# Kernel optimization log

Measured on AMD Instinct MI355X. Metric: run time of the kernel, lower is better.

Reference implementation:

```python
import jax, jax.numpy as jnp
import numpy as np

B, N, C = 4, 4096, 1024
H, D = 16, 64
EPS = 1e-6


def setup_inputs() -> dict:
    key = jax.random.key(0)
    ks = jax.random.split(key, 7)
    x = jax.random.normal(ks[0], (B, N, C), dtype=jnp.float32)
    # True = PAD (PyTorch convention)
    src_key_padding_mask = jax.random.randint(ks[1], (B, N), 0, 2).astype(jnp.bool_)
    s = 1.0 / np.sqrt(C)
    W_qkv = jax.random.uniform(ks[2], (3 * C, C), jnp.float32, -s, s)
    b_qkv = jax.random.uniform(ks[3], (3 * C,), jnp.float32, -s, s)
    W_out = jax.random.uniform(ks[4], (C, C), jnp.float32, -s, s)
    b_out = jax.random.uniform(ks[5], (C,), jnp.float32, -s, s)
    return {"x": x, "W_qkv": W_qkv, "b_qkv": b_qkv, "W_out": W_out,
            "b_out": b_out, "src_key_padding_mask": src_key_padding_mask}


def _phi(t):
    # elu(t) + 1  (alpha=1)
    return jnp.where(t > 0, t + 1.0, jnp.exp(t))


def reference(x, W_qkv, b_qkv, W_out, b_out, src_key_padding_mask):
    # qkv projection: [B,N,3C] -> [3,B,H,N,D]
    qkv = (x @ W_qkv.T + b_qkv).reshape(B, N, 3, H, D).transpose(2, 0, 3, 1, 4)
    q, k, v = qkv[0], qkv[1], qkv[2]
    qf = _phi(q)
    kf = _phi(k)
    valid = (~src_key_padding_mask).astype(kf.dtype)[:, None, :, None]  # [B,1,N,1]
    kf = kf * valid
    v = v * valid
    # kv state: [B,H,D,D]; z: [B,H,D]
    kv = jnp.einsum('bhnd,bhne->bhde', kf, v)
    z = kf.sum(axis=2)
    y_num = jnp.einsum('bhnd,bhde->bhne', qf, kv)      # [B,H,N,D]
    y_den = jnp.einsum('bhnd,bhd->bhn', qf, z)          # [B,H,N]
    y_den = jnp.maximum(y_den, EPS)[..., None]
    y = (y_num / y_den).transpose(0, 2, 1, 3).reshape(B, N, C)
    return y @ W_out.T + b_out
```

## Files before the change

### kernel.cpp

```cpp
#include <hip/hip_runtime.h>
#include <math.h>

#define B_ 4
#define N_ 4096
#define C_ 1024
#define H_ 16
#define D_ 64
#define M_ (B_*N_)
#define GK 1024
#define NCH 8
#define CHROWS (N_/NCH)

typedef __attribute__((ext_vector_type(8))) _Float16 f16x8;
typedef __attribute__((ext_vector_type(4))) _Float16 f16x4;
typedef __attribute__((ext_vector_type(4))) float f32x4;

__device__ __forceinline__ float phi_f(float t) {
  return (t > 0.0f) ? (t + 1.0f) : __expf(t);
}

#define GLOAD(gp, lp) __builtin_amdgcn_global_load_lds( \
    (const __attribute__((address_space(1))) unsigned int*)(gp), \
    (__attribute__((address_space(3))) unsigned int*)(lp), 16, 0, 0)

#define BAR() __builtin_amdgcn_s_barrier()
#define WAITL0() asm volatile("s_waitcnt lgkmcnt(0)" ::: "memory")
#define WAITV6() asm volatile("s_waitcnt vmcnt(6)" ::: "memory")
#define WAITV0() asm volatile("s_waitcnt vmcnt(0)" ::: "memory")
#define PRIO1() __builtin_amdgcn_s_setprio(1)
#define PRIO0() __builtin_amdgcn_s_setprio(0)

__device__ __forceinline__ f32x4 mfma16h(f16x8 a, f16x8 b, f32x4 c) {
  return __builtin_amdgcn_mfma_f32_16x16x32_f16(a, b, c, 0, 0, 0);
}

__global__ __launch_bounds__(256) void mask_detect_k(const unsigned int* __restrict__ w,
                                                     int* __restrict__ flag) {
  __shared__ int notint, notflt;
  if (threadIdx.x == 0) { notint = 0; notflt = 0; }
  __syncthreads();
  int ni = 0, nf = 0;
  for (int i = threadIdx.x; i < 4096; i += 256) {
    unsigned int v = w[i];
    if (v > 1u) ni = 1;
    if (v != 0u && v != 0x3F800000u) nf = 1;
  }
  if (ni) atomicOr(&notint, 1);
  if (nf) atomicOr(&notflt, 1);
  __syncthreads();
  if (threadIdx.x == 0) *flag = (!notint) ? 0 : ((!notflt) ? 1 : 2);
}

__global__ __launch_bounds__(256) void mask_convert_k(const void* __restrict__ mask,
                                                      const int* __restrict__ flag,
                                                      float* __restrict__ valid) {
  int i = blockIdx.x * 256 + threadIdx.x;
  int f = *flag;
  int m;
  if (f == 0)      m = ((const int*)mask)[i] != 0;
  else if (f == 1) m = ((const float*)mask)[i] != 0.0f;
  else             m = ((const unsigned char*)mask)[i] != 0;
  valid[i] = m ? 0.0f : 1.0f;
}

__global__ __launch_bounds__(256) void conv_f16_k(const float* __restrict__ src,
                                                  _Float16* __restrict__ dst, int n4) {
  int i = blockIdx.x * 256 + threadIdx.x;
  if (i >= n4) return;
  float4 v = ((const float4*)src)[i];
  f16x4 h;
  h[0] = (_Float16)v.x; h[1] = (_Float16)v.y;
  h[2] = (_Float16)v.z; h[3] = (_Float16)v.w;
  ((f16x4*)dst)[i] = h;
}

__global__ __launch_bounds__(256) void split_f16_k(const float* __restrict__ src,
                                                   _Float16* __restrict__ h,
                                                   _Float16* __restrict__ l, int n4) {
  int i = blockIdx.x * 256 + threadIdx.x;
  if (i >= n4) return;
  float4 v = ((const float4*)src)[i];
  f16x4 hv, lv;
  float vs[4] = {v.x, v.y, v.z, v.w};
#pragma unroll
  for (int q = 0; q < 4; ++q) {
    _Float16 hh = (_Float16)vs[q];
    _Float16 ll = (_Float16)(vs[q] - (float)hh);
    hv[q] = hh; lv[q] = ll;
  }
  ((f16x4*)h)[i] = hv;
  ((f16x4*)l)[i] = lv;
}

template <int EPI>
__global__ __launch_bounds__(512, 2) void gemm256_k(
    const _Float16* __restrict__ A,
    const _Float16* __restrict__ Bh, const _Float16* __restrict__ Bl,
    const float* __restrict__ bias, const float* __restrict__ valid,
    float* __restrict__ qf, float* __restrict__ kf, float* __restrict__ vv,
    float* __restrict__ outp, int jb, int jshift) {
  __shared__ _Float16 lds[73728];
  const int tid = threadIdx.x;
  const int lane = tid & 63, w = tid >> 6;
  const int lm = lane & 15, lq = lane >> 4;
  const int wm = w >> 2, wj = w & 3;

  const int nwg = gridDim.x;
  const int q8 = nwg >> 3;
  const int wid = (blockIdx.x & 7) * q8 + (blockIdx.x >> 3);
  const int j_blk = wid & ((1 << jshift) - 1);
  const int m_blk = wid >> jshift;
  const int m0 = m_blk * 256;
  const int jg0 = jb + j_blk * 256;

  const size_t gA0 = (size_t)(m0 + w * 16 + lm) * GK + lq * 8;
  const size_t gA1 = gA0 + (size_t)128 * GK;
  const size_t gB0 = (size_t)(jg0 + w * 16 + lm) * GK + lq * 8;
  const size_t gB1 = gB0 + (size_t)128 * GK;

#pragma unroll
  for (int tt = 0; tt < 2; ++tt) {
    _Float16* sq = lds + tt * 24576;
    const size_t ks = (size_t)tt * 32;
    GLOAD(A + gA0 + ks, sq + w * 512);
    GLOAD(A + gA1 + ks, sq + 4096 + w * 512);
    GLOAD(Bh + gB0 + ks, sq + 8192 + w * 512);
    GLOAD(Bh + gB1 + ks, sq + 12288 + w * 512);
    GLOAD(Bl + gB0 + ks, sq + 16384 + w * 512);
    GLOAD(Bl + gB1 + ks, sq + 20480 + w * 512);
  }
  WAITV6();
  BAR();

  f32x4 acc[8][4] = {};
  int pc = 0, ps = 2;
  for (int t = 0; t < 32; ++t) {
    const _Float16* bb = lds + pc * 24576;
    _Float16* sq = lds + ps * 24576;
    const bool st = (t + 2 < 32);
    const size_t ks = (size_t)(t + 2) * 32;
    f16x8 a0[4], a1[4], bh[4], bl[4];

#pragma unroll
    for (int i = 0; i < 4; ++i)
      a0[i] = *(const f16x8*)&bb[(wm * 8 + i) * 512 + lane * 8];
#pragma unroll
    for (int j = 0; j < 4; ++j)
      bh[j] = *(const f16x8*)&bb[8192 + (wj * 4 + j) * 512 + lane * 8];
    if (st) {
      GLOAD(A + gA0 + ks, sq + w * 512);
      GLOAD(A + gA1 + ks, sq + 4096 + w * 512);
    }
    BAR(); WAITL0();
    PRIO1();
#pragma unroll
    for (int i = 0; i < 4; ++i)
#pragma unroll
      for (int j = 0; j < 4; ++j)
        acc[i][j] = mfma16h(a0[i], bh[j], acc[i][j]);
    PRIO0(); BAR();

#pragma unroll
    for (int i = 0; i < 4; ++i)
      a1[i] = *(const f16x8*)&bb[(wm * 8 + 4 + i) * 512 + lane * 8];
    if (st) {
      GLOAD(Bh + gB0 + ks, sq + 8192 + w * 512);
      GLOAD(Bh + gB1 + ks, sq + 12288 + w * 512);
    }
    BAR(); WAITL0();
    PRIO1();
#pragma unroll
    for (int i = 0; i < 4; ++i)
#pragma unroll
      for (int j = 0; j < 4; ++j)
        acc[4 + i][j] = mfma16h(a1[i], bh[j], acc[4 + i][j]);
    PRIO0(); BAR();

#pragma unroll
    for (int j = 0; j < 4; ++j)
      bl[j] = *(const f16x8*)&bb[16384 + (wj * 4 + j) * 512 + lane * 8];
    if (st) {
      GLOAD(Bl + gB0 + ks, sq + 16384 + w * 512);
      GLOAD(Bl + gB1 + ks, sq + 20480 + w * 512);
    }
    BAR(); WAITL0();
    PRIO1();
#pragma unroll
    for (int i = 0; i < 4; ++i)
#pragma unroll
      for (int j = 0; j < 4; ++j)
        acc[i][j] = mfma16h(a0[i], bl[j], acc[i][j]);
    PRIO0(); BAR();

    PRIO1();
#pragma unroll
    for (int i = 0; i < 4; ++i)
#pragma unroll
      for (int j = 0; j < 4; ++j)
        acc[4 + i][j] = mfma16h(a1[i], bl[j], acc[4 + i][j]);
    PRIO0();
    if (t < 30)       { WAITV6(); }
    else if (t == 30) { WAITV0(); }
    if (t < 31) BAR();
    pc = (pc == 2) ? 0 : pc + 1;
    ps = (ps == 2) ? 0 : ps + 1;
  }

  if (EPI == 0) {
    const int ty = jg0 >> 10;
    float* dst = (ty == 0) ? qf : ((ty == 1) ? kf : vv);
    float vld[8][4];
#pragma unroll
    for (int i = 0; i < 8; ++i)
#pragma unroll
      for (int r = 0; r < 4; ++r)
        vld[i][r] = (ty == 0) ? 1.0f : valid[m0 + wm * 128 + i * 16 + lq * 4 + r];
#pragma unroll
    for (int jt = 0; jt < 4; ++jt) {
      int jcol = jg0 + wj * 64 + jt * 16 + lm;
      float bj = bias[jcol];
      int c = jcol & 1023, hd = c >> 6, d = c & 63;
#pragma unroll
      for (int i = 0; i < 8; ++i)
#pragma unroll
        for (int r = 0; r < 4; ++r) {
          int m = m0 + wm * 128 + i * 16 + lq * 4 + r;
          int b = m >> 12, n = m & 4095;
          float val = acc[i][jt][r] + bj;
          if (ty <= 1) val = phi_f(val);
          if (ty >= 1) val *= vld[i][r];
          dst[(((size_t)(b * H_ + hd) * N_ + n) << 6) + d] = val;
        }
    }
  } else {
#pragma unroll
    for (int jt = 0; jt < 4; ++jt) {
      int jcol = jg0 + wj * 64 + jt * 16 + lm;
      float bj = bias[jcol];
#pragma unroll
      for (int i = 0; i < 8; ++i)
#pragma unroll
        for (int r = 0; r < 4; ++r) {
          int m = m0 + wm * 128 + i * 16 + lq * 4 + r;
          outp[(size_t)m * C_ + jcol] = acc[i][jt][r] + bj;
        }
    }
  }
}

__global__ __launch_bounds__(256) void kv_partial_k(
    const float* __restrict__ kf, const float* __restrict__ vv,
    float* __restrict__ kvp, float* __restrict__ zp) {
  const int bh = blockIdx.x, ch = blockIdx.y;
  const float* kfr = kf + ((size_t)bh * N_ + ch * CHROWS) * 64;
  const float* vr  = vv + ((size_t)bh * N_ + ch * CHROWS) * 64;
  __shared__ float ks[8][64], vs[8][64];
  const int tid = threadIdx.x;
  const int d0 = tid >> 2, eg = tid & 3;
  float acc[16] = {};
  float zacc = 0.f;
  for (int nb = 0; nb < CHROWS; nb += 8) {
    {
      int which = tid >> 7;
      int fl = tid & 127;
      int rr = fl >> 4, cc = (fl & 15) * 4;
      const float* src = which ? vr : kfr;
      float4 t4 = *(const float4*)&src[(size_t)(nb + rr) * 64 + cc];
      float* d = which ? &vs[rr][cc] : &ks[rr][cc];
      *(float4*)d = t4;
    }
    __syncthreads();
#pragma unroll
    for (int r = 0; r < 8; ++r) {
      float kd = ks[r][d0];
      if (eg == 0) zacc += kd;
#pragma unroll
      for (int i = 0; i < 16; ++i) acc[i] += kd * vs[r][eg * 16 + i];
    }
    __syncthreads();
  }
  size_t base = ((size_t)bh * NCH + ch) * 4096 + (size_t)d0 * 64 + eg * 16;
#pragma unroll
  for (int i = 0; i < 16; i += 4)
    *(float4*)&kvp[base + i] = make_float4(acc[i], acc[i+1], acc[i+2], acc[i+3]);
  if (eg == 0) zp[((size_t)bh * NCH + ch) * 64 + d0] = zacc;
}

__global__ __launch_bounds__(256) void kv_reduce_k(
    const float* __restrict__ kvp, const float* __restrict__ zp,
    float* __restrict__ kv, float* __restrict__ z) {
  const int bh = blockIdx.x, tid = threadIdx.x;
  for (int i = tid; i < 4096; i += 256) {
    float s = 0.f;
#pragma unroll
    for (int c = 0; c < NCH; ++c) s += kvp[((size_t)bh * NCH + c) * 4096 + i];
    kv[(size_t)bh * 4096 + i] = s;
  }
  if (tid < 64) {
    float s = 0.f;
#pragma unroll
    for (int c = 0; c < NCH; ++c) s += zp[((size_t)bh * NCH + c) * 64 + tid];
    z[bh * 64 + tid] = s;
  }
}

__global__ __launch_bounds__(256) void attn_apply_k(
    const float* __restrict__ qf, const float* __restrict__ kv,
    const float* __restrict__ z, _Float16* __restrict__ Y) {
  const int bh = blockIdx.x, nt = blockIdx.y;
  const int b = bh >> 4, hd = bh & 15;
  __shared__ float qs[128][65];
  __shared__ float kvs[64][68];
  __shared__ float zs[64];
  __shared__ float dens[128];
  const int tid = threadIdx.x;
  const float* qrow = qf + ((size_t)bh * N_ + nt * 128) * 64;
#pragma unroll
  for (int i = 0; i < 4; ++i) {
    int fl = tid + i * 256;
    int d = fl >> 4, cc = (fl & 15) * 4;
    float4 t4 = *(const float4*)&kv[(size_t)bh * 4096 + d * 64 + cc];
    kvs[d][cc] = t4.x; kvs[d][cc+1] = t4.y; kvs[d][cc+2] = t4.z; kvs[d][cc+3] = t4.w;
  }
  if (tid < 64) zs[tid] = z[bh * 64 + tid];
#pragma unroll
  for (int i = 0; i < 8; ++i) {
    int fl = tid + i * 256;
    int r = fl >> 4, cc = (fl & 15) * 4;
    float4 t4 = *(const float4*)&qrow[(size_t)r * 64 + cc];
    qs[r][cc] = t4.x; qs[r][cc+1] = t4.y; qs[r][cc+2] = t4.z; qs[r][cc+3] = t4.w;
  }
  __syncthreads();
  {
    int n = tid >> 1, half = tid & 1;
    float s = 0.f;
#pragma unroll
    for (int dd = 0; dd < 32; ++dd) {
      int d = half * 32 + dd;
      s += qs[n][d] * zs[d];
    }
    float other = __shfl_down(s, 1);
    if (half == 0) dens[n] = fmaxf(s + other, 1e-6f);
  }
  __syncthreads();
  const int ng = tid >> 3, eg = tid & 7;
  float acc[4][8] = {};
  for (int d = 0; d < 64; ++d) {
    float kvrow[8];
    *(float4*)&kvrow[0] = *(const float4*)&kvs[d][eg * 8];
    *(float4*)&kvrow[4] = *(const float4*)&kvs[d][eg * 8 + 4];
#pragma unroll
    for (int i = 0; i < 4; ++i) {
      float a = qs[ng * 4 + i][d];
#pragma unroll
      for (int j = 0; j < 8; ++j) acc[i][j] += a * kvrow[j];
    }
  }
#pragma unroll
  for (int i = 0; i < 4; ++i) {
    int nl = ng * 4 + i;
    int n = nt * 128 + nl;
    float inv = 1.0f / dens[nl];
    size_t off = ((size_t)b * N_ + n) * C_ + hd * 64 + eg * 8;
    f16x8 hv;
#pragma unroll
    for (int j = 0; j < 8; ++j) hv[j] = (_Float16)(acc[i][j] * inv);
    *(f16x8*)&Y[off] = hv;
  }
}

extern "C" void kernel_launch(void* const* d_in, const int* in_sizes, int n_in,
                              void* d_out, int out_size, void* d_ws, size_t ws_size,
                              hipStream_t stream) {
  const float* x      = (const float*)d_in[0];
  const float* W_qkv  = (const float*)d_in[1];
  const float* b_qkv  = (const float*)d_in[2];
  const float* W_out  = (const float*)d_in[3];
  const float* b_out  = (const float*)d_in[4];
  const void*  mask   = d_in[5];
  float* out = (float*)d_out;

  const size_t bhnd = (size_t)B_ * H_ * N_ * D_;
  float* ws = (float*)d_ws;
  float* buf1 = ws;
  float* buf2 = ws + bhnd;
  _Float16* Xh  = (_Float16*)(ws + 2 * bhnd);
  _Float16* Wqh = Xh + bhnd;
  _Float16* Wql = Wqh + (size_t)3072 * 1024;
  _Float16* Woh = Wql + (size_t)3072 * 1024;
  _Float16* Wol = Woh + (size_t)1024 * 1024;
  float* tail2 = (float*)(Wol + (size_t)1024 * 1024);
  float* kvp = tail2;
  float* zp  = kvp + (size_t)64 * NCH * 4096;
  float* kv  = zp + (size_t)64 * NCH * 64;
  float* z   = kv + (size_t)64 * 4096;
  float* valid = z + 64 * 64;
  int*   flag  = (int*)(valid + M_);

  _Float16* Y = (_Float16*)buf2;

  mask_detect_k<<<1, 256, 0, stream>>>((const unsigned int*)mask, flag);
  mask_convert_k<<<M_ / 256, 256, 0, stream>>>(mask, flag, valid);
  conv_f16_k<<<(int)(bhnd / 4 / 256), 256, 0, stream>>>(x, Xh, (int)(bhnd / 4));
  split_f16_k<<<3072 * 1024 / 4 / 256, 256, 0, stream>>>(W_qkv, Wqh, Wql, 3072 * 1024 / 4);
  split_f16_k<<<1024 * 1024 / 4 / 256, 256, 0, stream>>>(W_out, Woh, Wol, 1024 * 1024 / 4);
  gemm256_k<0><<<512, 512, 0, stream>>>(
      Xh, Wqh, Wql, b_qkv, valid, buf1, buf1, buf2, nullptr, 1024, 3);
  kv_partial_k<<<dim3(B_ * H_, NCH), 256, 0, stream>>>(buf1, buf2, kvp, zp);
  kv_reduce_k<<<B_ * H_, 256, 0, stream>>>(kvp, zp, kv, z);
  gemm256_k<0><<<256, 512, 0, stream>>>(
      Xh, Wqh, Wql, b_qkv, valid, buf1, buf1, buf2, nullptr, 0, 2);
  attn_apply_k<<<dim3(B_ * H_, N_ / 128), 256, 0, stream>>>(buf1, kv, z, Y);
  gemm256_k<1><<<256, 512, 0, stream>>>(
      Y, Woh, Wol, b_out, valid, nullptr, nullptr, nullptr, out, 0, 2);
}
```

Before: 491.7 us.

## Restructure GEMM main loop with register prefetch and a single barrier per k-step

```diff
diff --git a/kernel.cpp b/kernel.cpp
--- a/kernel.cpp
+++ b/kernel.cpp
@@ -24,7 +24,7 @@
     (__attribute__((address_space(3))) unsigned int*)(lp), 16, 0, 0)
 
 #define BAR() __builtin_amdgcn_s_barrier()
-#define WAITL0() asm volatile("s_waitcnt lgkmcnt(0)" ::: "memory")
+#define SCHEDB() __builtin_amdgcn_sched_barrier(0)
 #define WAITV6() asm volatile("s_waitcnt vmcnt(6)" ::: "memory")
 #define WAITV0() asm volatile("s_waitcnt vmcnt(0)" ::: "memory")
 #define PRIO1() __builtin_amdgcn_s_setprio(1)
@@ -131,67 +131,82 @@
   }
   WAITV6();
   BAR();
+  SCHEDB();
 
   f32x4 acc[8][4] = {};
-  int pc = 0, ps = 2;
+  f16x8 a0[4], a1[4], bh[4], bl[4];
+#pragma unroll
+  for (int i = 0; i < 4; ++i)
+    a0[i] = *(const f16x8*)&lds[(wm * 8 + i) * 512 + lane * 8];
+#pragma unroll
+  for (int j = 0; j < 4; ++j)
+    bh[j] = *(const f16x8*)&lds[8192 + (wj * 4 + j) * 512 + lane * 8];
+
+  int pc = 0;
   for (int t = 0; t < 32; ++t) {
     const _Float16* bb = lds + pc * 24576;
-    _Float16* sq = lds + ps * 24576;
+    const int pn = (pc == 2) ? 0 : pc + 1;
+    const _Float16* nb = lds + pn * 24576;
+    const int psl = (pc == 0) ? 2 : pc - 1;
+    _Float16* sq = lds + psl * 24576;
     const bool st = (t + 2 < 32);
     const size_t ks = (size_t)(t + 2) * 32;
-    f16x8 a0[4], a1[4], bh[4], bl[4];
 
 #pragma unroll
     for (int i = 0; i < 4; ++i)
-      a0[i] = *(const f16x8*)&bb[(wm * 8 + i) * 512 + lane * 8];
+      a1[i] = *(const f16x8*)&bb[(wm * 8 + 4 + i) * 512 + lane * 8];
+    PRIO1();
+#pragma unroll
+    for (int i = 0; i < 4; ++i)
+#pragma unroll
+      for (int j = 0; j < 4; ++j)
+        acc[i][j] = mfma16h(a0[i], bh[j], acc[i][j]);
+    PRIO0();
+
 #pragma unroll
     for (int j = 0; j < 4; ++j)
-      bh[j] = *(const f16x8*)&bb[8192 + (wj * 4 + j) * 512 + lane * 8];
+      bl[j] = *(const f16x8*)&bb[16384 + (wj * 4 + j) * 512 + lane * 8];
+    PRIO1();
+#pragma unroll
+    for (int i = 0; i < 4; ++i)
+#pragma unroll
+      for (int j = 0; j < 4; ++j)
+        acc[4 + i][j] = mfma16h(a1[i], bh[j], acc[4 + i][j]);
+    PRIO0();
+
+    WAITV0();
+    BAR();
+    SCHEDB();
+
+    f16x8 a0n[4], bhn[4];
+    if (t < 31) {
+#pragma unroll
+      for (int i = 0; i < 4; ++i)
+        a0n[i] = *(const f16x8*)&nb[(wm * 8 + i) * 512 + lane * 8];
+    }
     if (st) {
       GLOAD(A + gA0 + ks, sq + w * 512);
       GLOAD(A + gA1 + ks, sq + 4096 + w * 512);
-    }
-    BAR(); WAITL0();
+      GLOAD(Bh + gB0 + ks, sq + 8192 + w * 512);
+    }
     PRIO1();
 #pragma unroll
     for (int i = 0; i < 4; ++i)
 #pragma unroll
       for (int j = 0; j < 4; ++j)
-        acc[i][j] = mfma16h(a0[i], bh[j], acc[i][j]);
-    PRIO0(); BAR();
-
-#pragma unroll
-    for (int i = 0; i < 4; ++i)
-      a1[i] = *(const f16x8*)&bb[(wm * 8 + 4 + i) * 512 + lane * 8];
+        acc[i][j] = mfma16h(a0[i], bl[j], acc[i][j]);
+    PRIO0();
+
+    if (t < 31) {
+#pragma unroll
+      for (int j = 0; j < 4; ++j)
+        bhn[j] = *(const f16x8*)&nb[8192 + (wj * 4 + j) * 512 + lane * 8];
+    }
     if (st) {
-      GLOAD(Bh + gB0 + ks, sq + 8192 + w * 512);
       GLOAD(Bh + gB1 + ks, sq + 12288 + w * 512);
-    }
-    BAR(); WAITL0();
-    PRIO1();
-#pragma unroll
-    for (int i = 0; i < 4; ++i)
-#pragma unroll
-      for (int j = 0; j < 4; ++j)
-        acc[4 + i][j] = mfma16h(a1[i], bh[j], acc[4 + i][j]);
-    PRIO0(); BAR();
-
-#pragma unroll
-    for (int j = 0; j < 4; ++j)
-      bl[j] = *(const f16x8*)&bb[16384 + (wj * 4 + j) * 512 + lane * 8];
-    if (st) {
       GLOAD(Bl + gB0 + ks, sq + 16384 + w * 512);
       GLOAD(Bl + gB1 + ks, sq + 20480 + w * 512);
     }
-    BAR(); WAITL0();
-    PRIO1();
-#pragma unroll
-    for (int i = 0; i < 4; ++i)
-#pragma unroll
-      for (int j = 0; j < 4; ++j)
-        acc[i][j] = mfma16h(a0[i], bl[j], acc[i][j]);
-    PRIO0(); BAR();
-
     PRIO1();
 #pragma unroll
     for (int i = 0; i < 4; ++i)
@@ -199,11 +214,12 @@
       for (int j = 0; j < 4; ++j)
         acc[4 + i][j] = mfma16h(a1[i], bl[j], acc[4 + i][j]);
     PRIO0();
-    if (t < 30)       { WAITV6(); }
-    else if (t == 30) { WAITV0(); }
-    if (t < 31) BAR();
-    pc = (pc == 2) ? 0 : pc + 1;
-    ps = (ps == 2) ? 0 : ps + 1;
+
+    if (t < 31) {
+#pragma unroll
+      for (int i = 0; i < 4; ++i) { a0[i] = a0n[i]; bh[i] = bhn[i]; }
+    }
+    pc = pn;
   }
 
   if (EPI == 0) {
```

Result: slower. 529.0 us (+7.6%).

## Software-pipeline GEMM LDS fragment loads across k-tiles and unroll the triple-buffer ring

Applied to the files above, without the earlier changes.

```diff
diff --git a/kernel.cpp b/kernel.cpp
--- a/kernel.cpp
+++ b/kernel.cpp
@@ -23,9 +23,9 @@
     (const __attribute__((address_space(1))) unsigned int*)(gp), \
     (__attribute__((address_space(3))) unsigned int*)(lp), 16, 0, 0)
 
-#define BAR() __builtin_amdgcn_s_barrier()
-#define WAITL0() asm volatile("s_waitcnt lgkmcnt(0)" ::: "memory")
+#define BARM() asm volatile("s_barrier" ::: "memory")
 #define WAITV6() asm volatile("s_waitcnt vmcnt(6)" ::: "memory")
+#define WAITV4() asm volatile("s_waitcnt vmcnt(4)" ::: "memory")
 #define WAITV0() asm volatile("s_waitcnt vmcnt(0)" ::: "memory")
 #define PRIO1() __builtin_amdgcn_s_setprio(1)
 #define PRIO0() __builtin_amdgcn_s_setprio(0)
@@ -91,6 +91,58 @@
   ((f16x4*)h)[i] = hv;
   ((f16x4*)l)[i] = lv;
 }
+
+
+#define TILE_BODY(PC, DO_STAGE, DO_PRE, WAITK, KS)                             \
+  {                                                                            \
+    const _Float16* bb = lds + (PC) * 24576;                                   \
+    const _Float16* nb = lds + (((PC) + 1) % 3) * 24576;                       \
+    _Float16* sq = lds + (((PC) + 2) % 3) * 24576;                             \
+    const size_t ks = (KS);                                                    \
+                                     \
+    _Pragma("unroll") for (int j = 0; j < 4; ++j)                              \
+      bl[j] = *(const f16x8*)&bb[16384 + (wj * 4 + j) * 512 + lane * 8];       \
+    if (DO_STAGE) { GLOAD(A + gA0 + ks, sq + w * 512);                         \
+                    GLOAD(A + gA1 + ks, sq + 4096 + w * 512); }                \
+    BARM();                                                                    \
+    PRIO1();                                                                   \
+    _Pragma("unroll") for (int i = 0; i < 4; ++i)                              \
+      _Pragma("unroll") for (int j = 0; j < 4; ++j)                            \
+        acc[i][j] = mfma16h(a0[i], bh[j], acc[i][j]);                          \
+    PRIO0();                                                                   \
+        \
+    _Pragma("unroll") for (int i = 0; i < 4; ++i)                              \
+      a1[i] = *(const f16x8*)&bb[(wm * 8 + 4 + i) * 512 + lane * 8];           \
+    if (DO_STAGE) { GLOAD(Bh + gB0 + ks, sq + 8192 + w * 512);                 \
+                    GLOAD(Bh + gB1 + ks, sq + 12288 + w * 512); }              \
+    if ((WAITK) == 1) { WAITV4(); } else if ((WAITK) == 2) { WAITV0(); }       \
+    BARM();                                                                    \
+    PRIO1();                                                                   \
+    _Pragma("unroll") for (int i = 0; i < 4; ++i)                              \
+      _Pragma("unroll") for (int j = 0; j < 4; ++j)                            \
+        acc[i][j] = mfma16h(a0[i], bl[j], acc[i][j]);                          \
+    PRIO0();                                                                   \
+                                \
+    if (DO_PRE) { _Pragma("unroll") for (int i = 0; i < 4; ++i)                \
+      a0[i] = *(const f16x8*)&nb[(wm * 8 + i) * 512 + lane * 8]; }             \
+    if (DO_STAGE) { GLOAD(Bl + gB0 + ks, sq + 16384 + w * 512);                \
+                    GLOAD(Bl + gB1 + ks, sq + 20480 + w * 512); }              \
+    BARM();                                                                    \
+    PRIO1();                                                                   \
+    _Pragma("unroll") for (int i = 0; i < 4; ++i)                              \
+      _Pragma("unroll") for (int j = 0; j < 4; ++j)                            \
+        acc[4 + i][j] = mfma16h(a1[i], bh[j], acc[4 + i][j]);                  \
+    PRIO0();                                                                   \
+                                          \
+    if (DO_PRE) { _Pragma("unroll") for (int j = 0; j < 4; ++j)                \
+      bh[j] = *(const f16x8*)&nb[8192 + (wj * 4 + j) * 512 + lane * 8]; }      \
+    BARM();                                                                    \
+    PRIO1();                                                                   \
+    _Pragma("unroll") for (int i = 0; i < 4; ++i)                              \
+      _Pragma("unroll") for (int j = 0; j < 4; ++j)                            \
+        acc[4 + i][j] = mfma16h(a1[i], bl[j], acc[4 + i][j]);                  \
+    PRIO0();                                                                   \
+  }
 
 template <int EPI>
 __global__ __launch_bounds__(512, 2) void gemm256_k(
@@ -130,81 +182,25 @@
     GLOAD(Bl + gB1 + ks, sq + 20480 + w * 512);
   }
   WAITV6();
-  BAR();
+  BARM();
 
   f32x4 acc[8][4] = {};
-  int pc = 0, ps = 2;
-  for (int t = 0; t < 32; ++t) {
-    const _Float16* bb = lds + pc * 24576;
-    _Float16* sq = lds + ps * 24576;
-    const bool st = (t + 2 < 32);
-    const size_t ks = (size_t)(t + 2) * 32;
-    f16x8 a0[4], a1[4], bh[4], bl[4];
-
-#pragma unroll
-    for (int i = 0; i < 4; ++i)
-      a0[i] = *(const f16x8*)&bb[(wm * 8 + i) * 512 + lane * 8];
-#pragma unroll
-    for (int j = 0; j < 4; ++j)
-      bh[j] = *(const f16x8*)&bb[8192 + (wj * 4 + j) * 512 + lane * 8];
-    if (st) {
-      GLOAD(A + gA0 + ks, sq + w * 512);
-      GLOAD(A + gA1 + ks, sq + 4096 + w * 512);
-    }
-    BAR(); WAITL0();
-    PRIO1();
-#pragma unroll
-    for (int i = 0; i < 4; ++i)
-#pragma unroll
-      for (int j = 0; j < 4; ++j)
-        acc[i][j] = mfma16h(a0[i], bh[j], acc[i][j]);
-    PRIO0(); BAR();
-
-#pragma unroll
-    for (int i = 0; i < 4; ++i)
-      a1[i] = *(const f16x8*)&bb[(wm * 8 + 4 + i) * 512 + lane * 8];
-    if (st) {
-      GLOAD(Bh + gB0 + ks, sq + 8192 + w * 512);
-      GLOAD(Bh + gB1 + ks, sq + 12288 + w * 512);
-    }
-    BAR(); WAITL0();
-    PRIO1();
-#pragma unroll
-    for (int i = 0; i < 4; ++i)
-#pragma unroll
-      for (int j = 0; j < 4; ++j)
-        acc[4 + i][j] = mfma16h(a1[i], bh[j], acc[4 + i][j]);
-    PRIO0(); BAR();
-
-#pragma unroll
-    for (int j = 0; j < 4; ++j)
-      bl[j] = *(const f16x8*)&bb[16384 + (wj * 4 + j) * 512 + lane * 8];
-    if (st) {
-      GLOAD(Bl + gB0 + ks, sq + 16384 + w * 512);
-      GLOAD(Bl + gB1 + ks, sq + 20480 + w * 512);
-    }
-    BAR(); WAITL0();
-    PRIO1();
-#pragma unroll
-    for (int i = 0; i < 4; ++i)
-#pragma unroll
-      for (int j = 0; j < 4; ++j)
-        acc[i][j] = mfma16h(a0[i], bl[j], acc[i][j]);
-    PRIO0(); BAR();
-
-    PRIO1();
-#pragma unroll
-    for (int i = 0; i < 4; ++i)
-#pragma unroll
-      for (int j = 0; j < 4; ++j)
-        acc[4 + i][j] = mfma16h(a1[i], bl[j], acc[4 + i][j]);
-    PRIO0();
-    if (t < 30)       { WAITV6(); }
-    else if (t == 30) { WAITV0(); }
-    if (t < 31) BAR();
-    pc = (pc == 2) ? 0 : pc + 1;
-    ps = (ps == 2) ? 0 : ps + 1;
-  }
+  f16x8 a0[4], a1[4], bh[4], bl[4];
+#pragma unroll
+  for (int i = 0; i < 4; ++i)
+    a0[i] = *(const f16x8*)&lds[(wm * 8 + i) * 512 + lane * 8];
+#pragma unroll
+  for (int j = 0; j < 4; ++j)
+    bh[j] = *(const f16x8*)&lds[8192 + (wj * 4 + j) * 512 + lane * 8];
+
+  for (int it = 0; it < 10; ++it) {
+    const int t0 = 3 * it;
+    TILE_BODY(0, true, true, 1, (size_t)(t0 + 2) * 32)
+    TILE_BODY(1, true, true, 1, (size_t)(t0 + 3) * 32)
+    TILE_BODY(2, true, true, 1, (size_t)(t0 + 4) * 32)
+  }
+  TILE_BODY(0, false, true, 2, 0)
+  TILE_BODY(1, false, false, 0, 0)
 
   if (EPI == 0) {
     const int ty = jg0 >> 10;
```

Result: no change. 493.8 us (+0.4%).
